# Optimization experiments

Hardware: AMD Instinct MI355X
Metric: run time of the kernel (lower is better)

Reference implementation:

```python
import jax, jax.numpy as jnp
import numpy as np

B, LQ, LK, DQ, DKEY, DV = 8, 2048, 2048, 1024, 1024, 1024
MASK_NEG = -1e6  # d2l masked_softmax fill value


def setup_inputs() -> dict:
    key = jax.random.key(0)
    kq, kk, kv, kl, kw = jax.random.split(key, 5)
    queries = jax.random.normal(kq, (B, LQ, DQ), dtype=jnp.float32)
    keys = jax.random.normal(kk, (B, LK, DKEY), dtype=jnp.float32)
    values = jax.random.normal(kv, (B, LK, DV), dtype=jnp.float32)
    valid_lens = jax.random.randint(kl, (B,), 1, LK + 1)
    W_q = jax.random.normal(kw, (DQ, DKEY), dtype=jnp.float32) / np.sqrt(DQ)
    return {"queries": queries, "keys": keys, "values": values,
            "valid_lens": valid_lens, "W_q": W_q}


def reference(queries, keys, values, valid_lens, W_q):
    # Q projection: LazyLinear(key_dim, bias=False)
    q = jnp.einsum("bqd,dk->bqk", queries, W_q)          # [B, LQ, DKEY]
    d = q.shape[-1]
    scores = jnp.einsum("bqk,bsk->bqs", q, keys) / jnp.sqrt(jnp.asarray(d, q.dtype))
    # masked_softmax: positions >= valid_len set to -1e6 before softmax
    mask = jnp.arange(scores.shape[-1])[None, None, :] < valid_lens[:, None, None]
    scores = jnp.where(mask, scores, MASK_NEG)
    attn = jax.nn.softmax(scores, axis=-1)               # [B, LQ, LK]
    # dropout p=0.0 (eval) -> identity
    return jnp.einsum("bqs,bsv->bqv", attn, values)      # [B, LQ, DV]
```

## Files before the change

kernel.cpp:

```cpp
#include <hip/hip_runtime.h>
#include <cstdint>
#include <cstddef>

#define B_   8
#define LQ_  2048
#define LK_  2048

typedef __attribute__((ext_vector_type(8))) __bf16 bf16x8;
typedef __attribute__((ext_vector_type(4))) float f32x4;
typedef __attribute__((ext_vector_type(8))) unsigned short ushortx8;

__device__ __forceinline__ unsigned short f2bf(float f) {
  unsigned u = __builtin_bit_cast(unsigned, f);
  u = u + 0x7fffu + ((u >> 16) & 1u);
  return (unsigned short)(u >> 16);
}
__device__ __forceinline__ float bf2f(unsigned short h) {
  unsigned u = ((unsigned)h) << 16;
  return __builtin_bit_cast(float, u);
}

__device__ __forceinline__ void gld_lds16(const void* g, void* l) {
  __builtin_amdgcn_global_load_lds((__attribute__((address_space(1))) void*)(void*)g,
                                   (__attribute__((address_space(3))) void*)l, 16, 0, 0);
}

__global__ __launch_bounds__(256) void cast_kw_kernel(
    const float* __restrict__ k, unsigned short* __restrict__ ko,
    const float* __restrict__ w, unsigned short* __restrict__ wo,
    const int* __restrict__ vlp) {
  int bb = (int)blockIdx.x;
  const float* in;
  unsigned short* out;
  if (bb < 8192) {
    in = k; out = ko;
    int batch = bb >> 10;
    int row = (bb & 1023) * 2;
    int vl = vlp[batch];
    if (row >= ((vl + 255) & ~255)) return;
  } else {
    bb -= 8192;
    in = w; out = wo;
  }
  size_t i = ((size_t)bb * 256 + threadIdx.x) * 8;
  float4 a = *(const float4*)(in + i);
  float4 b = *(const float4*)(in + i + 4);
  ushortx8 o;
  o[0] = f2bf(a.x); o[1] = f2bf(a.y); o[2] = f2bf(a.z); o[3] = f2bf(a.w);
  o[4] = f2bf(b.x); o[5] = f2bf(b.y); o[6] = f2bf(b.z); o[7] = f2bf(b.w);
  *(ushortx8*)(out + i) = o;
}

template <int OUTM, int SKIPN, int SKIPM, int CLAMPK, int AUX>
__global__ __launch_bounds__(256, 2) void gemm256x128_kernel(
    const unsigned short* __restrict__ A, const unsigned short* __restrict__ B,
    void* __restrict__ Cp, int M, int N, int K,
    long a_bstride, long b_bstride, long c_bstride, float scale,
    const int* __restrict__ vlp, int lognx,
    const float* __restrict__ auxf, unsigned short* __restrict__ auxo, int ngemm) {
  __shared__ unsigned short lds[2][128 * 64 + 64 * 64];

  const int tid = threadIdx.x;

  if constexpr (AUX == 1) {
    if ((int)blockIdx.x >= ngemm) {
      size_t i = ((size_t)((int)blockIdx.x - ngemm) * 256 + tid) * 8;
      float4 a = *(const float4*)(auxf + i);
      float4 b = *(const float4*)(auxf + i + 4);
      ushortx8 o;
      o[0] = f2bf(a.x); o[1] = f2bf(a.y); o[2] = f2bf(a.z); o[3] = f2bf(a.w);
      o[4] = f2bf(b.x); o[5] = f2bf(b.y); o[6] = f2bf(b.z); o[7] = f2bf(b.w);
      *(ushortx8*)(auxo + i) = o;
      return;
    }
  }
  if constexpr (AUX == 2) {
    if ((int)blockIdx.x >= ngemm) {
      float* smem = (float*)&lds[0][0];
      const int vb = (int)blockIdx.x - ngemm;
      const int tx = tid & 31, ty = tid >> 5;
#pragma unroll 1
      for (int u = 0; u < 8; ++u) {
        const int t = vb * 8 + u;
        const int z = t >> 11;
        const int r0 = ((t >> 5) & 63) * 32;
        const int c0 = (t & 31) * 32;
        const int kEnd = (vlp[z] + 63) & ~63;
        if (r0 < kEnd) {
          const float* inb = auxf + (size_t)z * 2048 * 1024;
          unsigned short* outb = auxo + (size_t)z * 1024 * 2048;
#pragma unroll
          for (int k = 0; k < 4; ++k) {
            int r = ty + k * 8;
            smem[r * 33 + tx] = inb[(size_t)(r0 + r) * 1024 + c0 + tx];
          }
          __syncthreads();
#pragma unroll
          for (int k = 0; k < 4; ++k) {
            int c = ty + k * 8;
            outb[(size_t)(c0 + c) * 2048 + r0 + tx] = f2bf(smem[tx * 33 + c]);
          }
          __syncthreads();
        }
      }
      return;
    }
  }

  const int wid = tid >> 6;
  const int lane = tid & 63;
  const int lane15 = lane & 15;
  const int lhalf = lane >> 4;

  const int idx = (int)blockIdx.x;
  const int z = idx & 7;
  const int rest = idx >> 3;
  const int nxm = (1 << lognx) - 1;
  const int xt = rest & nxm;
  const int yt = rest >> lognx;
  const int nt = (xt + 2 * z) & nxm;
  const int m0 = yt * 256;
  const int n0 = nt * 128;

  int vl = K;
  if constexpr (SKIPN || SKIPM || CLAMPK) vl = vlp[z];
  if constexpr (SKIPN) {
    if (n0 >= vl) return;
  }
  if constexpr (SKIPM) {
    if (m0 >= vl) return;
  }
  int kEnd = K;
  if constexpr (CLAMPK) {
    int ke = (vl + 63) & ~63;
    kEnd = ke < K ? ke : K;
  }
  const int nKt = kEnd >> 5;

  const unsigned short* Ab = A + (size_t)z * a_bstride;
  const unsigned short* Bb = B + (size_t)z * b_bstride;

  int srA[4], scA[4], sdA[4];
#pragma unroll
  for (int j = 0; j < 4; ++j) {
    int blk = (wid * 4 + j) * 64 + lane;
    int p = blk >> 3;
    int c = (blk & 7) ^ (p & 7);
    srA[j] = m0 + 2 * p + (c >> 2);
    scA[j] = (c & 3) * 8;
    sdA[j] = blk * 8;
  }
  int srB[2], scB[2], sdB[2];
#pragma unroll
  for (int j = 0; j < 2; ++j) {
    int blk = (wid * 2 + j) * 64 + lane;
    int p = blk >> 3;
    int c = (blk & 7) ^ (p & 7);
    srB[j] = n0 + 2 * p + (c >> 2);
    scB[j] = (c & 3) * 8;
    sdB[j] = 8192 + blk * 8;
  }

  const int om = (wid & 1) * 128;
  const int on = (wid >> 1) * 64;
  const int swz8 = ((((lane15 & 1) << 2) + lhalf) ^ ((lane15 >> 1) & 7)) << 3;
  const int aBase = ((om >> 1) + (lane15 >> 1)) * 64 + swz8;
  const int bBase = 8192 + ((on >> 1) + (lane15 >> 1)) * 64 + swz8;

  f32x4 acc[8][4];
#pragma unroll
  for (int f = 0; f < 8; ++f)
#pragma unroll
    for (int g = 0; g < 4; ++g) acc[f][g] = (f32x4){0.f, 0.f, 0.f, 0.f};

#define STAGE_TILE(T, S)                                                        \
  {                                                                             \
    const int kc_ = (T) * 32;                                                   \
    _Pragma("unroll")                                                           \
    for (int j = 0; j < 4; ++j)                                                 \
      gld_lds16(Ab + (size_t)srA[j] * K + (kc_ + scA[j]), &lds[S][sdA[j]]);     \
    _Pragma("unroll")                                                           \
    for (int j = 0; j < 2; ++j)                                                 \
      gld_lds16(Bb + (size_t)srB[j] * K + (kc_ + scB[j]), &lds[S][sdB[j]]);     \
  }

  STAGE_TILE(0, 0);
  asm volatile("s_waitcnt vmcnt(0)" ::: "memory");
  __builtin_amdgcn_s_barrier();

  for (int t = 0; t < nKt; ++t) {
    const unsigned short* lcur = &lds[t & 1][0];
    if (t + 1 < nKt) STAGE_TILE(t + 1, (t + 1) & 1);

    bf16x8 a[8], b[4];
#pragma unroll
    for (int f = 0; f < 8; ++f) a[f] = *(const bf16x8*)&lcur[aBase + f * 512];
#pragma unroll
    for (int g = 0; g < 4; ++g) b[g] = *(const bf16x8*)&lcur[bBase + g * 512];
#pragma unroll
    for (int f = 0; f < 8; ++f)
#pragma unroll
      for (int g = 0; g < 4; ++g)
        acc[f][g] = __builtin_amdgcn_mfma_f32_16x16x32_bf16(a[f], b[g], acc[f][g], 0, 0, 0);
    asm volatile("s_waitcnt vmcnt(0)" ::: "memory");
    __builtin_amdgcn_s_barrier();
  }
#undef STAGE_TILE

  const size_t boffC = (size_t)z * c_bstride;
#pragma unroll
  for (int f = 0; f < 8; ++f) {
    int row = m0 + om + f * 16 + lhalf * 4;
#pragma unroll
    for (int g = 0; g < 4; ++g) {
      int col = n0 + on + g * 16 + lane15;
#pragma unroll
      for (int r = 0; r < 4; ++r) {
        float v = acc[f][g][r];
        if constexpr (OUTM == 0) {
          ((unsigned short*)Cp + boffC)[(size_t)(row + r) * N + col] = f2bf(v);
        } else if constexpr (OUTM == 1) {
          ((unsigned short*)Cp + boffC)[(size_t)(row + r) * N + col] = f2bf(v * scale);
        } else {
          ((float*)Cp + boffC)[(size_t)(row + r) * N + col] = v;
        }
      }
    }
  }
}

__global__ __launch_bounds__(256) void softmax_kernel(unsigned short* __restrict__ scores,
                                                      const int* __restrict__ valid_lens) {
  const int row = blockIdx.x;
  const int b = row >> 11;
  const int vl = valid_lens[b];
  const int kEnd = (vl + 63) & ~63;
  unsigned short* rp = scores + (size_t)row * LK_;
  const int tid = threadIdx.x;
  const int wid = tid >> 6, lane = tid & 63;
  __shared__ float sred[4];

  const int cb = tid * 8;
  const bool act = cb < kEnd;
  ushortx8 h = {};
  if (act) h = *(const ushortx8*)(rp + cb);
  float x[8];
#pragma unroll
  for (int t = 0; t < 8; ++t) x[t] = bf2f(h[t]);

  float m = -3.4e38f;
#pragma unroll
  for (int t = 0; t < 8; ++t)
    if (cb + t < vl) m = fmaxf(m, x[t]);
#pragma unroll
  for (int off = 32; off >= 1; off >>= 1) m = fmaxf(m, __shfl_xor(m, off));
  if (lane == 0) sred[wid] = m;
  __syncthreads();
  m = fmaxf(fmaxf(sred[0], sred[1]), fmaxf(sred[2], sred[3]));
  __syncthreads();

  float e[8];
  float s = 0.f;
#pragma unroll
  for (int t = 0; t < 8; ++t) {
    e[t] = (cb + t < vl) ? __expf(x[t] - m) : 0.f;
    s += e[t];
  }
#pragma unroll
  for (int off = 32; off >= 1; off >>= 1) s += __shfl_xor(s, off);
  if (lane == 0) sred[wid] = s;
  __syncthreads();
  s = sred[0] + sred[1] + sred[2] + sred[3];
  float inv = 1.f / s;

  if (act) {
    ushortx8 o;
#pragma unroll
    for (int t = 0; t < 8; ++t) o[t] = f2bf(e[t] * inv);
    *(ushortx8*)(rp + cb) = o;
  }
}

extern "C" void kernel_launch(void* const* d_in, const int* in_sizes, int n_in,
                              void* d_out, int out_size, void* d_ws, size_t ws_size,
                              hipStream_t stream) {
  const float* queries = (const float*)d_in[0];
  const float* keys = (const float*)d_in[1];
  const float* values = (const float*)d_in[2];
  const int* valid_lens = (const int*)d_in[3];
  const float* W_q = (const float*)d_in[4];
  float* out = (float*)d_out;

  unsigned short* ws = (unsigned short*)d_ws;
  const size_t M1 = (size_t)1024 * 1024;
  unsigned short* q_bf = ws;
  unsigned short* scores = ws + 16 * M1;
  unsigned short* keysP = ws + 48 * M1;
  unsigned short* w_bf = ws + 64 * M1;
  unsigned short* keys_bf = ws + 65 * M1;
  unsigned short* valsT = keys_bf;

  cast_kw_kernel<<<dim3(8704), 256, 0, stream>>>(
      keys, keys_bf, W_q, w_bf, valid_lens);
  gemm256x128_kernel<0, 0, 1, 0, 1><<<dim3(512 + 8192), 256, 0, stream>>>(
      keys_bf, w_bf, keysP, 2048, 1024, 1024,
      (long)2048 * 1024, 0, (long)2048 * 1024, 1.f, valid_lens, 3,
      queries, q_bf, 512);
  gemm256x128_kernel<1, 1, 0, 0, 2><<<dim3(1024 + 2048), 256, 0, stream>>>(
      q_bf, keysP, scores, 2048, 2048, 1024,
      (long)2048 * 1024, (long)2048 * 1024, (long)2048 * 2048, 0.03125f, valid_lens, 4,
      values, valsT, 1024);
  softmax_kernel<<<dim3(B_ * LQ_), 256, 0, stream>>>(scores, valid_lens);
  gemm256x128_kernel<2, 0, 0, 1, 0><<<dim3(8 * 8 * 8), 256, 0, stream>>>(
      scores, valsT, out, 2048, 1024, 2048,
      (long)2048 * 2048, (long)1024 * 2048, (long)2048 * 1024, 1.f, valid_lens, 3,
      nullptr, nullptr, 0);
}
```

Measured before the change: 371.3 us.

## Fuse fp32-to-bf16 casts into GEMM staging and split-K the final PV GEMM

Removes the separate cast kernel. The first GEMM now reads fp32 keys and W_q directly, converting them to bf16 in registers before the LDS writes. The values transpose-cast moves into the first GEMM's aux blocks so it runs concurrently, and the softmax kernel also zeroes the output for batches with long valid lengths. The final attention-times-V GEMM then splits K in two and accumulates with float atomics. This trades extra register pressure and the loss of async global-to-LDS loads in GEMM1 for fewer kernel launches, fewer global round trips, and more parallelism on the last GEMM.

```diff
diff --git a/kernel.cpp b/kernel.cpp
--- a/kernel.cpp
+++ b/kernel.cpp
@@ -25,82 +25,57 @@
                                    (__attribute__((address_space(3))) void*)l, 16, 0, 0);
 }
 
-__global__ __launch_bounds__(256) void cast_kw_kernel(
-    const float* __restrict__ k, unsigned short* __restrict__ ko,
-    const float* __restrict__ w, unsigned short* __restrict__ wo,
-    const int* __restrict__ vlp) {
-  int bb = (int)blockIdx.x;
-  const float* in;
-  unsigned short* out;
-  if (bb < 8192) {
-    in = k; out = ko;
-    int batch = bb >> 10;
-    int row = (bb & 1023) * 2;
-    int vl = vlp[batch];
-    if (row >= ((vl + 255) & ~255)) return;
-  } else {
-    bb -= 8192;
-    in = w; out = wo;
-  }
-  size_t i = ((size_t)bb * 256 + threadIdx.x) * 8;
-  float4 a = *(const float4*)(in + i);
-  float4 b = *(const float4*)(in + i + 4);
-  ushortx8 o;
-  o[0] = f2bf(a.x); o[1] = f2bf(a.y); o[2] = f2bf(a.z); o[3] = f2bf(a.w);
-  o[4] = f2bf(b.x); o[5] = f2bf(b.y); o[6] = f2bf(b.z); o[7] = f2bf(b.w);
-  *(ushortx8*)(out + i) = o;
-}
-
-template <int OUTM, int SKIPN, int SKIPM, int CLAMPK, int AUX>
+template <int OUTM, int SKIPN, int SKIPM, int CLAMPK, int AUX, int STGF32, int SPLITK>
 __global__ __launch_bounds__(256, 2) void gemm256x128_kernel(
     const unsigned short* __restrict__ A, const unsigned short* __restrict__ B,
     void* __restrict__ Cp, int M, int N, int K,
     long a_bstride, long b_bstride, long c_bstride, float scale,
     const int* __restrict__ vlp, int lognx,
-    const float* __restrict__ auxf, unsigned short* __restrict__ auxo, int ngemm) {
+    const float* __restrict__ auxf, unsigned short* __restrict__ auxo,
+    const float* __restrict__ auxf2, unsigned short* __restrict__ auxo2,
+    int ngemm) {
   __shared__ unsigned short lds[2][128 * 64 + 64 * 64];
 
   const int tid = threadIdx.x;
 
-  if constexpr (AUX == 1) {
-    if ((int)blockIdx.x >= ngemm) {
-      size_t i = ((size_t)((int)blockIdx.x - ngemm) * 256 + tid) * 8;
-      float4 a = *(const float4*)(auxf + i);
-      float4 b = *(const float4*)(auxf + i + 4);
-      ushortx8 o;
-      o[0] = f2bf(a.x); o[1] = f2bf(a.y); o[2] = f2bf(a.z); o[3] = f2bf(a.w);
-      o[4] = f2bf(b.x); o[5] = f2bf(b.y); o[6] = f2bf(b.z); o[7] = f2bf(b.w);
-      *(ushortx8*)(auxo + i) = o;
-      return;
-    }
-  }
-  if constexpr (AUX == 2) {
-    if ((int)blockIdx.x >= ngemm) {
-      float* smem = (float*)&lds[0][0];
-      const int vb = (int)blockIdx.x - ngemm;
-      const int tx = tid & 31, ty = tid >> 5;
+  if constexpr (AUX) {
+    const int bi = (int)blockIdx.x - ngemm;
+    if (bi >= 0) {
+      if (bi < 8192) {
+        size_t i = ((size_t)bi * 256 + tid) * 8;
+        float4 a = *(const float4*)(auxf + i);
+        float4 b = *(const float4*)(auxf + i + 4);
+        ushortx8 o;
+        o[0] = f2bf(a.x); o[1] = f2bf(a.y); o[2] = f2bf(a.z); o[3] = f2bf(a.w);
+        o[4] = f2bf(b.x); o[5] = f2bf(b.y); o[6] = f2bf(b.z); o[7] = f2bf(b.w);
+        *(ushortx8*)(auxo + i) = o;
+      } else {
+        float* smem = (float*)&lds[0][0];
+        const int vb = bi - 8192;
+        const int tx = tid & 31, ty = tid >> 5;
 #pragma unroll 1
-      for (int u = 0; u < 8; ++u) {
-        const int t = vb * 8 + u;
-        const int z = t >> 11;
-        const int r0 = ((t >> 5) & 63) * 32;
-        const int c0 = (t & 31) * 32;
-        const int kEnd = (vlp[z] + 63) & ~63;
-        if (r0 < kEnd) {
-          const float* inb = auxf + (size_t)z * 2048 * 1024;
-          unsigned short* outb = auxo + (size_t)z * 1024 * 2048;
-#pragma unroll
-          for (int k = 0; k < 4; ++k) {
-            int r = ty + k * 8;
-            smem[r * 33 + tx] = inb[(size_t)(r0 + r) * 1024 + c0 + tx];
+        for (int u = 0; u < 8; ++u) {
+          const int t = vb * 8 + u;
+          const int z = t >> 11;
+          const int r0 = ((t >> 5) & 63) * 32;
+          const int c0 = (t & 31) * 32;
+          const int ke = (vlp[z] + 63) & ~63;
+          if (r0 < ke) {
+            const float* inb = auxf2 + (size_t)z * 2048 * 1024;
+            unsigned short* outb = auxo2 + (size_t)z * 1024 * 2048;
+#pragma unroll
+            for (int k = 0; k < 4; ++k) {
+              int r = ty + k * 8;
+              smem[r * 33 + tx] = inb[(size_t)(r0 + r) * 1024 + c0 + tx];
+            }
+            __syncthreads();
+#pragma unroll
+            for (int k = 0; k < 4; ++k) {
+              int c = ty + k * 8;
+              outb[(size_t)(c0 + c) * 2048 + r0 + tx] = f2bf(smem[tx * 33 + c]);
+            }
+            __syncthreads();
           }
-          __syncthreads();
-#pragma unroll
-          for (int k = 0; k < 4; ++k) {
-            int c = ty + k * 8;
-            outb[(size_t)(c0 + c) * 2048 + r0 + tx] = f2bf(smem[tx * 33 + c]);
-          }
-          __syncthreads();
         }
       }
       return;
@@ -114,7 +89,12 @@
 
   const int idx = (int)blockIdx.x;
   const int z = idx & 7;
-  const int rest = idx >> 3;
+  int rest = idx >> 3;
+  int sk = 0;
+  if constexpr (SPLITK) {
+    sk = rest & 1;
+    rest >>= 1;
+  }
   const int nxm = (1 << lognx) - 1;
   const int xt = rest & nxm;
   const int yt = rest >> lognx;
@@ -137,8 +117,17 @@
   }
   const int nKt = kEnd >> 5;
 
-  const unsigned short* Ab = A + (size_t)z * a_bstride;
-  const unsigned short* Bb = B + (size_t)z * b_bstride;
+  int t0 = 0, t1 = nKt;
+  bool split = false;
+  if constexpr (SPLITK) {
+    if (nKt >= 32) {
+      split = true;
+      const int h = nKt >> 1;
+      if (sk) t0 = h; else t1 = h;
+    } else if (sk) {
+      return;
+    }
+  }
 
   int srA[4], scA[4], sdA[4];
 #pragma unroll
@@ -173,6 +162,77 @@
 #pragma unroll
     for (int g = 0; g < 4; ++g) acc[f][g] = (f32x4){0.f, 0.f, 0.f, 0.f};
 
+  if constexpr (STGF32) {
+    const float* Af = (const float*)(const void*)A + (size_t)z * a_bstride;
+    const float* Bf = (const float*)(const void*)B + (size_t)z * b_bstride;
+    float4 pa[4][2], pb[2][2];
+
+#define LOADF(T)                                                                \
+  {                                                                             \
+    const int kc_ = (T) * 32;                                                   \
+    _Pragma("unroll")                                                           \
+    for (int j = 0; j < 4; ++j) {                                               \
+      const float* s = Af + (size_t)srA[j] * K + (kc_ + scA[j]);                \
+      pa[j][0] = *(const float4*)s;                                             \
+      pa[j][1] = *(const float4*)(s + 4);                                       \
+    }                                                                           \
+    _Pragma("unroll")                                                           \
+    for (int j = 0; j < 2; ++j) {                                               \
+      const float* s = Bf + (size_t)srB[j] * K + (kc_ + scB[j]);                \
+      pb[j][0] = *(const float4*)s;                                             \
+      pb[j][1] = *(const float4*)(s + 4);                                       \
+    }                                                                           \
+  }
+#define WRITEF(S)                                                               \
+  {                                                                             \
+    _Pragma("unroll")                                                           \
+    for (int j = 0; j < 4; ++j) {                                               \
+      ushortx8 o;                                                               \
+      o[0] = f2bf(pa[j][0].x); o[1] = f2bf(pa[j][0].y);                         \
+      o[2] = f2bf(pa[j][0].z); o[3] = f2bf(pa[j][0].w);                         \
+      o[4] = f2bf(pa[j][1].x); o[5] = f2bf(pa[j][1].y);                         \
+      o[6] = f2bf(pa[j][1].z); o[7] = f2bf(pa[j][1].w);                         \
+      *(ushortx8*)&lds[S][sdA[j]] = o;                                          \
+    }                                                                           \
+    _Pragma("unroll")                                                           \
+    for (int j = 0; j < 2; ++j) {                                               \
+      ushortx8 o;                                                               \
+      o[0] = f2bf(pb[j][0].x); o[1] = f2bf(pb[j][0].y);                         \
+      o[2] = f2bf(pb[j][0].z); o[3] = f2bf(pb[j][0].w);                         \
+      o[4] = f2bf(pb[j][1].x); o[5] = f2bf(pb[j][1].y);                         \
+      o[6] = f2bf(pb[j][1].z); o[7] = f2bf(pb[j][1].w);                         \
+      *(ushortx8*)&lds[S][sdB[j]] = o;                                          \
+    }                                                                           \
+  }
+
+    LOADF(t0);
+    WRITEF(0);
+    __syncthreads();
+    for (int t = t0; t < t1; ++t) {
+      const int cur = (t - t0) & 1;
+      const unsigned short* lcur = &lds[cur][0];
+      if (t + 1 < t1) LOADF(t + 1);
+
+      bf16x8 a[8], b[4];
+#pragma unroll
+      for (int f = 0; f < 8; ++f) a[f] = *(const bf16x8*)&lcur[aBase + f * 512];
+#pragma unroll
+      for (int g = 0; g < 4; ++g) b[g] = *(const bf16x8*)&lcur[bBase + g * 512];
+#pragma unroll
+      for (int f = 0; f < 8; ++f)
+#pragma unroll
+        for (int g = 0; g < 4; ++g)
+          acc[f][g] = __builtin_amdgcn_mfma_f32_16x16x32_bf16(a[f], b[g], acc[f][g], 0, 0, 0);
+
+      if (t + 1 < t1) WRITEF(cur ^ 1);
+      __syncthreads();
+    }
+#undef LOADF
+#undef WRITEF
+  } else {
+    const unsigned short* Ab = A + (size_t)z * a_bstride;
+    const unsigned short* Bb = B + (size_t)z * b_bstride;
+
 #define STAGE_TILE(T, S)                                                        \
   {                                                                             \
     const int kc_ = (T) * 32;                                                   \
@@ -184,28 +244,30 @@
       gld_lds16(Bb + (size_t)srB[j] * K + (kc_ + scB[j]), &lds[S][sdB[j]]);     \
   }
 
-  STAGE_TILE(0, 0);
-  asm volatile("s_waitcnt vmcnt(0)" ::: "memory");
-  __builtin_amdgcn_s_barrier();
-
-  for (int t = 0; t < nKt; ++t) {
-    const unsigned short* lcur = &lds[t & 1][0];
-    if (t + 1 < nKt) STAGE_TILE(t + 1, (t + 1) & 1);
-
-    bf16x8 a[8], b[4];
-#pragma unroll
-    for (int f = 0; f < 8; ++f) a[f] = *(const bf16x8*)&lcur[aBase + f * 512];
-#pragma unroll
-    for (int g = 0; g < 4; ++g) b[g] = *(const bf16x8*)&lcur[bBase + g * 512];
-#pragma unroll
-    for (int f = 0; f < 8; ++f)
-#pragma unroll
-      for (int g = 0; g < 4; ++g)
-        acc[f][g] = __builtin_amdgcn_mfma_f32_16x16x32_bf16(a[f], b[g], acc[f][g], 0, 0, 0);
+    STAGE_TILE(t0, 0);
     asm volatile("s_waitcnt vmcnt(0)" ::: "memory");
     __builtin_amdgcn_s_barrier();
-  }
+
+    for (int t = t0; t < t1; ++t) {
+      const int cur = (t - t0) & 1;
+      const unsigned short* lcur = &lds[cur][0];
+      if (t + 1 < t1) STAGE_TILE(t + 1, cur ^ 1);
+
+      bf16x8 a[8], b[4];
+#pragma unroll
+      for (int f = 0; f < 8; ++f) a[f] = *(const bf16x8*)&lcur[aBase + f * 512];
+#pragma unroll
+      for (int g = 0; g < 4; ++g) b[g] = *(const bf16x8*)&lcur[bBase + g * 512];
+#pragma unroll
+      for (int f = 0; f < 8; ++f)
+#pragma unroll
+        for (int g = 0; g < 4; ++g)
+          acc[f][g] = __builtin_amdgcn_mfma_f32_16x16x32_bf16(a[f], b[g], acc[f][g], 0, 0, 0);
+      asm volatile("s_waitcnt vmcnt(0)" ::: "memory");
+      __builtin_amdgcn_s_barrier();
+    }
 #undef STAGE_TILE
+  }
 
   const size_t boffC = (size_t)z * c_bstride;
 #pragma unroll
@@ -222,21 +284,44 @@
         } else if constexpr (OUTM == 1) {
           ((unsigned short*)Cp + boffC)[(size_t)(row + r) * N + col] = f2bf(v * scale);
         } else {
-          ((float*)Cp + boffC)[(size_t)(row + r) * N + col] = v;
+          float* op = (float*)Cp + boffC;
+          if constexpr (SPLITK) {
+            if (split) {
+              __hip_atomic_fetch_add(&op[(size_t)(row + r) * N + col], v,
+                                     __ATOMIC_RELAXED, __HIP_MEMORY_SCOPE_AGENT);
+              continue;
+            }
+          }
+          op[(size_t)(row + r) * N + col] = v;
         }
       }
     }
   }
 }
 
-__global__ __launch_bounds__(256) void softmax_kernel(unsigned short* __restrict__ scores,
-                                                      const int* __restrict__ valid_lens) {
-  const int row = blockIdx.x;
+__global__ __launch_bounds__(256) void softmax_zero_kernel(
+    unsigned short* __restrict__ scores, const int* __restrict__ valid_lens,
+    float* __restrict__ out) {
+  const int bb = (int)blockIdx.x;
+  const int tid = threadIdx.x;
+
+  if (bb >= 16384) {
+    const int zb = bb - 16384;
+    const int z = zb >> 8;
+    if (((valid_lens[z] + 63) & ~63) >= 1024) {
+      float* p = out + ((size_t)z << 21) + ((size_t)(zb & 255) << 13) + tid * 32;
+      const f32x4 zer = {0.f, 0.f, 0.f, 0.f};
+#pragma unroll
+      for (int u = 0; u < 8; ++u) *(f32x4*)(p + u * 4) = zer;
+    }
+    return;
+  }
+
+  const int row = bb;
   const int b = row >> 11;
   const int vl = valid_lens[b];
   const int kEnd = (vl + 63) & ~63;
   unsigned short* rp = scores + (size_t)row * LK_;
-  const int tid = threadIdx.x;
   const int wid = tid >> 6, lane = tid & 63;
   __shared__ float sred[4];
 
@@ -296,23 +381,20 @@
   unsigned short* q_bf = ws;
   unsigned short* scores = ws + 16 * M1;
   unsigned short* keysP = ws + 48 * M1;
-  unsigned short* w_bf = ws + 64 * M1;
-  unsigned short* keys_bf = ws + 65 * M1;
-  unsigned short* valsT = keys_bf;
-
-  cast_kw_kernel<<<dim3(8704), 256, 0, stream>>>(
-      keys, keys_bf, W_q, w_bf, valid_lens);
-  gemm256x128_kernel<0, 0, 1, 0, 1><<<dim3(512 + 8192), 256, 0, stream>>>(
-      keys_bf, w_bf, keysP, 2048, 1024, 1024,
+  unsigned short* valsT = ws + 64 * M1;
+
+  gemm256x128_kernel<0, 0, 1, 0, 1, 1, 0><<<dim3(512 + 8192 + 2048), 256, 0, stream>>>(
+      (const unsigned short*)(const void*)keys, (const unsigned short*)(const void*)W_q,
+      keysP, 2048, 1024, 1024,
       (long)2048 * 1024, 0, (long)2048 * 1024, 1.f, valid_lens, 3,
-      queries, q_bf, 512);
-  gemm256x128_kernel<1, 1, 0, 0, 2><<<dim3(1024 + 2048), 256, 0, stream>>>(
+      queries, q_bf, values, valsT, 512);
+  gemm256x128_kernel<1, 1, 0, 0, 0, 0, 0><<<dim3(8 * 16 * 8), 256, 0, stream>>>(
       q_bf, keysP, scores, 2048, 2048, 1024,
       (long)2048 * 1024, (long)2048 * 1024, (long)2048 * 2048, 0.03125f, valid_lens, 4,
-      values, valsT, 1024);
-  softmax_kernel<<<dim3(B_ * LQ_), 256, 0, stream>>>(scores, valid_lens);
-  gemm256x128_kernel<2, 0, 0, 1, 0><<<dim3(8 * 8 * 8), 256, 0, stream>>>(
+      nullptr, nullptr, nullptr, nullptr, 0);
+  softmax_zero_kernel<<<dim3(16384 + 2048), 256, 0, stream>>>(scores, valid_lens, out);
+  gemm256x128_kernel<2, 0, 0, 1, 0, 0, 1><<<dim3(8 * 8 * 2 * 8), 256, 0, stream>>>(
       scores, valsT, out, 2048, 1024, 2048,
       (long)2048 * 2048, (long)1024 * 2048, (long)2048 * 1024, 1.f, valid_lens, 3,
-      nullptr, nullptr, 0);
-}
+      nullptr, nullptr, nullptr, nullptr, 0);
+}
```

New measurement: 451.1 us. 1.21x slower.
